# Kernel optimization log

Measured on AMD Instinct MI355X. Metric: run time of the kernel, lower is better.

## Reference

```python
import jax, jax.numpy as jnp
import numpy as np

B, S, D, E, K = 4, 4096, 4096, 64, 2
TEMP = 1.0  # temperature=1.0 -> scale by 1/temperature kept for faithfulness


def setup_inputs() -> dict:
    key = jax.random.key(0)
    k1, k2 = jax.random.split(key)
    x = jax.random.normal(k1, (B, S, D), dtype=jnp.float32)
    W_gate = jax.random.normal(k2, (E, D), dtype=jnp.float32) * (D ** -0.5)
    return {"x": x, "W_gate": W_gate}


def reference(x, W_gate):
    # gate: Linear(d_model, n_experts, bias=False) -> logits [B,S,E]
    logits = jnp.einsum('bsd,ed->bse', x, W_gate)
    # temperature scaling (eval mode: no jitter / expert dropout / gumbel)
    logits = logits * (1.0 / TEMP)
    probs_full = jax.nn.softmax(logits, axis=-1)           # [B,S,E]
    topk_vals, idx = jax.lax.top_k(logits, K)              # [B,S,K]
    scores = jax.nn.softmax(topk_vals, axis=-1)            # renormalized top-k gates
    # z-loss: mean(logsumexp(logits)^2)
    z = jax.nn.logsumexp(logits, axis=-1)                  # [B,S]
    z_loss = jnp.mean(z * z)
    # aux stats (computed under no_grad in the original)
    importance = jax.lax.stop_gradient(jnp.mean(probs_full, axis=(0, 1)))  # [E]
    idx_flat = idx.reshape(-1)
    counts = jnp.zeros((E,), probs_full.dtype).at[idx_flat].add(1.0)       # [E]
    load = jax.lax.stop_gradient(counts / jnp.maximum(jnp.sum(counts), 1.0))
    return (idx, scores, probs_full, z_loss, importance, load)
```

## Files before the change

kernel.cpp:

```cpp
#include <hip/hip_runtime.h>

namespace {
constexpr int D = 4096;
constexpr int E = 64;
constexpr int M = 16384;
constexpr int BM = 64;
constexpr int BK = 64;
constexpr int NT = D / BK;
constexpr int NBLK = M / BM;

constexpr int OFF_IDX = 0;
constexpr int OFF_SCORES = 32768;
constexpr int OFF_PROBS = 65536;
constexpr int OFF_Z = 1114112;
constexpr int OFF_IMP = 1114113;
constexpr int OFF_LOAD = 1114177;

constexpr int WS_STRIDE = 132;
}

__global__ __launch_bounds__(512, 2) void router_fused(
    const float* __restrict__ xg, const float* __restrict__ wg,
    float* __restrict__ out, float* __restrict__ ws) {
  __shared__ float smem[16384];

  const int t = threadIdx.x;
  const int u = t & 127;
  const int s = t >> 7;
  const int tx = u & 15;
  const int ty = u >> 4;
  const int r0 = blockIdx.x * BM;

  const int sr = t >> 3;
  const int sc = (t & 7) * 4;
  const float* xp = xg + (size_t)(r0 + sr) * D + sc;
  const float* wp = wg + (size_t)sr * D + sc;

  float4 vx[2], vw[2];

  auto stage_load = [&](int k0) {
    vx[0] = *(const float4*)(xp + k0);
    vx[1] = *(const float4*)(xp + k0 + 32);
    vw[0] = *(const float4*)(wp + k0);
    vw[1] = *(const float4*)(wp + k0 + 32);
  };
  auto stage_write = [&](float* buf) {
    float* Xs = buf;
    float* Ws = buf + 4096;
#pragma unroll
    for (int h = 0; h < 2; ++h) {
      const int c = sc + h * 32;
      const int sw = ((c >> 4) & 3) << 3;
      const int rp = sr ^ sw;
      Xs[(c + 0) * 64 + rp] = vx[h].x;
      Xs[(c + 1) * 64 + rp] = vx[h].y;
      Xs[(c + 2) * 64 + rp] = vx[h].z;
      Xs[(c + 3) * 64 + rp] = vx[h].w;
      Ws[(c + 0) * 64 + rp] = vw[h].x;
      Ws[(c + 1) * 64 + rp] = vw[h].y;
      Ws[(c + 2) * 64 + rp] = vw[h].z;
      Ws[(c + 3) * 64 + rp] = vw[h].w;
    }
  };

  float acc[8][4];
#pragma unroll
  for (int i = 0; i < 8; ++i)
#pragma unroll
    for (int j = 0; j < 4; ++j) acc[i][j] = 0.f;

  const int rbx = (ty * 8) ^ (s << 3);
  const int rbw = (tx * 4) ^ (s << 3);

  stage_load(0);
  stage_write(smem);

  for (int r = 0; r < NT; ++r) {
    __syncthreads();
    if (r + 1 < NT) stage_load((r + 1) * BK);

    const float* buf = smem + (r & 1) * 8192;
    const float* Xs = buf + (size_t)(s * 16) * 64;
    const float* Ws = buf + 4096 + (size_t)(s * 16) * 64;
#pragma unroll
    for (int kk = 0; kk < 16; ++kk) {
      const float4 a0 = *(const float4*)&Xs[kk * 64 + rbx];
      const float4 a1 = *(const float4*)&Xs[kk * 64 + rbx + 4];
      const float4 bw = *(const float4*)&Ws[kk * 64 + rbw];
      const float av[8] = {a0.x, a0.y, a0.z, a0.w, a1.x, a1.y, a1.z, a1.w};
      const float bv[4] = {bw.x, bw.y, bw.z, bw.w};
#pragma unroll
      for (int i = 0; i < 8; ++i)
#pragma unroll
        for (int j = 0; j < 4; ++j) acc[i][j] = fmaf(av[i], bv[j], acc[i][j]);
    }
    if (r + 1 < NT) stage_write(smem + ((r + 1) & 1) * 8192);
  }

  float* P = smem;
  __syncthreads();
  if (s >= 2) {
    float* p = P + ((size_t)((s - 2) * 128 + u)) * 33;
#pragma unroll
    for (int i = 0; i < 8; ++i)
#pragma unroll
      for (int j = 0; j < 4; ++j) p[i * 4 + j] = acc[i][j];
  }
  __syncthreads();
  if (s < 2) {
    const float* p = P + ((size_t)(s * 128 + u)) * 33;
#pragma unroll
    for (int i = 0; i < 8; ++i)
#pragma unroll
      for (int j = 0; j < 4; ++j) acc[i][j] += p[i * 4 + j];
  }
  __syncthreads();
  if (s == 1) {
    float* p = P + (size_t)u * 33;
#pragma unroll
    for (int i = 0; i < 8; ++i)
#pragma unroll
      for (int j = 0; j < 4; ++j) p[i * 4 + j] = acc[i][j];
  }
  __syncthreads();

  float* Lg = smem + 8448;
  float* rowmax = smem + 12608;
  float* rowrs = rowmax + 64;
  float* zrow = rowrs + 64;
  int* cnt = (int*)(zrow + 64);

  if (s == 0) {
    const float* p = P + (size_t)u * 33;
#pragma unroll
    for (int i = 0; i < 8; ++i)
#pragma unroll
      for (int j = 0; j < 4; ++j) {
        const float v = acc[i][j] + p[i * 4 + j];
        Lg[(ty * 8 + i) * 65 + tx * 4 + j] = v;
      }
  }
  if (t < 64) cnt[t] = 0;
  __syncthreads();

  if (t < 64) {
    const float* row = Lg + t * 65;
    float v1 = -3.402823466e+38f, v2 = -3.402823466e+38f;
    int i1 = 0, i2 = 0;
#pragma unroll 8
    for (int e = 0; e < 64; ++e) {
      const float x = row[e];
      if (x > v1) {
        v2 = v1; i2 = i1; v1 = x; i1 = e;
      } else if (x > v2) {
        v2 = x; i2 = e;
      }
    }
    float ssum = 0.f;
#pragma unroll 8
    for (int e = 0; e < 64; ++e) ssum += __expf(row[e] - v1);
    const float z = v1 + __logf(ssum);
    rowmax[t] = v1;
    rowrs[t] = 1.f / ssum;
    zrow[t] = z * z;

    const int r = r0 + t;
    out[OFF_IDX + 2 * r] = (float)i1;
    out[OFF_IDX + 2 * r + 1] = (float)i2;
    const float e1 = __expf(v2 - v1);
    const float s0 = 1.f / (1.f + e1);
    out[OFF_SCORES + 2 * r] = s0;
    out[OFF_SCORES + 2 * r + 1] = e1 * s0;
    atomicAdd(&cnt[i1], 1);
    atomicAdd(&cnt[i2], 1);
  }
  __syncthreads();

  {
    const int pr = t >> 3;
    const int pc = (t & 7) * 8;
    float* prow = Lg + pr * 65 + pc;
    const float m = rowmax[pr];
    const float rs = rowrs[pr];
    float p[8];
#pragma unroll
    for (int q = 0; q < 8; ++q) p[q] = __expf(prow[q] - m) * rs;
    float4 o0 = {p[0], p[1], p[2], p[3]};
    float4 o1 = {p[4], p[5], p[6], p[7]};
    *(float4*)&out[OFF_PROBS + (size_t)(r0 + pr) * 64 + pc] = o0;
    *(float4*)&out[OFF_PROBS + (size_t)(r0 + pr) * 64 + pc + 4] = o1;
#pragma unroll
    for (int q = 0; q < 8; ++q) prow[q] = p[q];
  }
  __syncthreads();

  if (t < 64) {
    float ic = 0.f;
#pragma unroll 8
    for (int rr = 0; rr < 64; ++rr) ic += Lg[rr * 65 + t];
    ws[(size_t)blockIdx.x * WS_STRIDE + t] = ic;
    ws[(size_t)blockIdx.x * WS_STRIDE + 64 + t] = (float)cnt[t];
    float zz = zrow[t];
#pragma unroll
    for (int off = 32; off > 0; off >>= 1) zz += __shfl_xor(zz, off);
    if (t == 0) ws[(size_t)blockIdx.x * WS_STRIDE + 128] = zz;
  }
}

__global__ __launch_bounds__(192) void router_reduce(
    const float* __restrict__ ws, float* __restrict__ out) {
  const int t = threadIdx.x;
  if (t < 129) {
    float v = 0.f;
#pragma unroll 8
    for (int b = 0; b < NBLK; ++b) v += ws[(size_t)b * WS_STRIDE + t];
    if (t < 64)
      out[OFF_IMP + t] = v * (1.f / 16384.f);
    else if (t < 128)
      out[OFF_LOAD + (t - 64)] = v * (1.f / 32768.f);
    else
      out[OFF_Z] = v * (1.f / 16384.f);
  }
}

extern "C" void kernel_launch(void* const* d_in, const int* in_sizes, int n_in,
                              void* d_out, int out_size, void* d_ws, size_t ws_size,
                              hipStream_t stream) {
  const float* x = (const float*)d_in[0];
  const float* wgate = (const float*)d_in[1];
  float* out = (float*)d_out;
  float* ws = (float*)d_ws;

  router_fused<<<dim3(NBLK), dim3(512), 0, stream>>>(x, wgate, out, ws);
  router_reduce<<<dim3(1), dim3(192), 0, stream>>>(ws, out);
}
```

Baseline: 409.1 us.

## Double BK, use 8x8 per-thread tiles with 8-way split-K and warp-level epilogue

Doubles the K tile to 128 and raises shared memory to 128 KB. Each thread now computes an 8x8 register tile, with eight K-slices reduced through shared memory. This cuts barriers per K step and the LDS traffic per FMA. The epilogue moves to shuffle-based top-2/softmax across 8 lanes per row instead of serial per-row loops, and the final reduce kernel is parallelized across 512 threads. The larger shared memory footprint likely limits blocks per CU below the requested two, lowering occupancy.

```diff
diff --git a/kernel.cpp b/kernel.cpp
--- a/kernel.cpp
+++ b/kernel.cpp
@@ -5,7 +5,7 @@
 constexpr int E = 64;
 constexpr int M = 16384;
 constexpr int BM = 64;
-constexpr int BK = 64;
+constexpr int BK = 128;
 constexpr int NT = D / BK;
 constexpr int NBLK = M / BM;
 
@@ -22,55 +22,47 @@
 __global__ __launch_bounds__(512, 2) void router_fused(
     const float* __restrict__ xg, const float* __restrict__ wg,
     float* __restrict__ out, float* __restrict__ ws) {
-  __shared__ float smem[16384];
+  __shared__ float smem[32768];
 
   const int t = threadIdx.x;
-  const int u = t & 127;
-  const int s = t >> 7;
-  const int tx = u & 15;
-  const int ty = u >> 4;
+  const int u = t & 63;
+  const int s = t >> 6;
+  const int tx = u & 7;
+  const int ty = u >> 3;
   const int r0 = blockIdx.x * BM;
 
   const int sr = t >> 3;
   const int sc = (t & 7) * 4;
   const float* xp = xg + (size_t)(r0 + sr) * D + sc;
   const float* wp = wg + (size_t)sr * D + sc;
-
-  float4 vx[2], vw[2];
-
+  const int rp = sr ^ ((t & 7) << 2);
+
+  float4 vx[4], vw[4];
   auto stage_load = [&](int k0) {
-    vx[0] = *(const float4*)(xp + k0);
-    vx[1] = *(const float4*)(xp + k0 + 32);
-    vw[0] = *(const float4*)(wp + k0);
-    vw[1] = *(const float4*)(wp + k0 + 32);
+#pragma unroll
+    for (int h = 0; h < 4; ++h) {
+      vx[h] = *(const float4*)(xp + k0 + h * 32);
+      vw[h] = *(const float4*)(wp + k0 + h * 32);
+    }
   };
   auto stage_write = [&](float* buf) {
-    float* Xs = buf;
-    float* Ws = buf + 4096;
-#pragma unroll
-    for (int h = 0; h < 2; ++h) {
-      const int c = sc + h * 32;
-      const int sw = ((c >> 4) & 3) << 3;
-      const int rp = sr ^ sw;
-      Xs[(c + 0) * 64 + rp] = vx[h].x;
-      Xs[(c + 1) * 64 + rp] = vx[h].y;
-      Xs[(c + 2) * 64 + rp] = vx[h].z;
-      Xs[(c + 3) * 64 + rp] = vx[h].w;
-      Ws[(c + 0) * 64 + rp] = vw[h].x;
-      Ws[(c + 1) * 64 + rp] = vw[h].y;
-      Ws[(c + 2) * 64 + rp] = vw[h].z;
-      Ws[(c + 3) * 64 + rp] = vw[h].w;
+#pragma unroll
+    for (int h = 0; h < 4; ++h) {
+      float* px = buf + (sc + h * 32) * 64 + rp;
+      px[0] = vx[h].x; px[64] = vx[h].y; px[128] = vx[h].z; px[192] = vx[h].w;
+      float* pw = px + 8192;
+      pw[0] = vw[h].x; pw[64] = vw[h].y; pw[128] = vw[h].z; pw[192] = vw[h].w;
     }
   };
 
-  float acc[8][4];
+  float acc[8][8];
 #pragma unroll
   for (int i = 0; i < 8; ++i)
 #pragma unroll
-    for (int j = 0; j < 4; ++j) acc[i][j] = 0.f;
-
-  const int rbx = (ty * 8) ^ (s << 3);
-  const int rbw = (tx * 4) ^ (s << 3);
+    for (int j = 0; j < 8; ++j) acc[i][j] = 0.f;
+
+  const int rxs = (ty * 8) ^ ((s & 1) << 4);
+  const int rws = (tx * 8) ^ ((s & 1) << 4);
 
   stage_load(0);
   stage_write(smem);
@@ -79,147 +71,181 @@
     __syncthreads();
     if (r + 1 < NT) stage_load((r + 1) * BK);
 
-    const float* buf = smem + (r & 1) * 8192;
-    const float* Xs = buf + (size_t)(s * 16) * 64;
-    const float* Ws = buf + 4096 + (size_t)(s * 16) * 64;
+    const float* buf = smem + (r & 1) * 16384;
+    const float* Xs = buf + s * 1024;
+    const float* Ws = buf + 8192 + s * 1024;
 #pragma unroll
     for (int kk = 0; kk < 16; ++kk) {
-      const float4 a0 = *(const float4*)&Xs[kk * 64 + rbx];
-      const float4 a1 = *(const float4*)&Xs[kk * 64 + rbx + 4];
-      const float4 bw = *(const float4*)&Ws[kk * 64 + rbw];
+      const int vb = (kk >> 2) << 2;
+      const int px = rxs ^ vb;
+      const int pw = rws ^ vb;
+      const float4 a0 = *(const float4*)&Xs[kk * 64 + px];
+      const float4 a1 = *(const float4*)&Xs[kk * 64 + (px ^ 4)];
+      const float4 b0 = *(const float4*)&Ws[kk * 64 + pw];
+      const float4 b1 = *(const float4*)&Ws[kk * 64 + (pw ^ 4)];
       const float av[8] = {a0.x, a0.y, a0.z, a0.w, a1.x, a1.y, a1.z, a1.w};
-      const float bv[4] = {bw.x, bw.y, bw.z, bw.w};
+      const float bv[8] = {b0.x, b0.y, b0.z, b0.w, b1.x, b1.y, b1.z, b1.w};
 #pragma unroll
       for (int i = 0; i < 8; ++i)
 #pragma unroll
-        for (int j = 0; j < 4; ++j) acc[i][j] = fmaf(av[i], bv[j], acc[i][j]);
-    }
-    if (r + 1 < NT) stage_write(smem + ((r + 1) & 1) * 8192);
-  }
-
-  float* P = smem;
-  __syncthreads();
-  if (s >= 2) {
-    float* p = P + ((size_t)((s - 2) * 128 + u)) * 33;
+        for (int j = 0; j < 8; ++j) acc[i][j] = fmaf(av[i], bv[j], acc[i][j]);
+    }
+    if (r + 1 < NT) stage_write(smem + ((r + 1) & 1) * 16384);
+  }
+
+  __syncthreads();
+  {
+    float* P = smem;
+    const int su2 = (s * 64 + u) * 2;
 #pragma unroll
     for (int i = 0; i < 8; ++i)
 #pragma unroll
-      for (int j = 0; j < 4; ++j) p[i * 4 + j] = acc[i][j];
-  }
-  __syncthreads();
-  if (s < 2) {
-    const float* p = P + ((size_t)(s * 128 + u)) * 33;
-#pragma unroll
-    for (int i = 0; i < 8; ++i)
-#pragma unroll
-      for (int j = 0; j < 4; ++j) acc[i][j] += p[i * 4 + j];
-  }
-  __syncthreads();
-  if (s == 1) {
-    float* p = P + (size_t)u * 33;
-#pragma unroll
-    for (int i = 0; i < 8; ++i)
-#pragma unroll
-      for (int j = 0; j < 4; ++j) p[i * 4 + j] = acc[i][j];
-  }
-  __syncthreads();
-
-  float* Lg = smem + 8448;
-  float* rowmax = smem + 12608;
-  float* rowrs = rowmax + 64;
-  float* zrow = rowrs + 64;
-  int* cnt = (int*)(zrow + 64);
-
-  if (s == 0) {
-    const float* p = P + (size_t)u * 33;
-#pragma unroll
-    for (int i = 0; i < 8; ++i)
-#pragma unroll
-      for (int j = 0; j < 4; ++j) {
-        const float v = acc[i][j] + p[i * 4 + j];
-        Lg[(ty * 8 + i) * 65 + tx * 4 + j] = v;
+      for (int jj = 0; jj < 4; ++jj)
+        *(float2*)&P[(i * 4 + jj) * 1024 + su2] =
+            make_float2(acc[i][2 * jj], acc[i][2 * jj + 1]);
+  }
+  __syncthreads();
+
+  float v[8];
+#pragma unroll
+  for (int q = 0; q < 8; ++q) v[q] = 0.f;
+  {
+    const float* P = smem;
+#pragma unroll
+    for (int sl = 0; sl < 8; ++sl)
+#pragma unroll
+      for (int qq = 0; qq < 4; ++qq) {
+        const float2 f =
+            *(const float2*)&P[(s * 4 + qq) * 1024 + (sl * 64 + u) * 2];
+        v[2 * qq] += f.x;
+        v[2 * qq + 1] += f.y;
       }
   }
+  const int row = (u >> 3) * 8 + s;
+  const int ebase = (u & 7) * 8;
+  const int gr = r0 + row;
+
+  __syncthreads();
+  float* PW = smem;
+  float* zw = smem + 512;
+  int* cnt = (int*)(smem + 520);
   if (t < 64) cnt[t] = 0;
   __syncthreads();
 
-  if (t < 64) {
-    const float* row = Lg + t * 65;
-    float v1 = -3.402823466e+38f, v2 = -3.402823466e+38f;
-    int i1 = 0, i2 = 0;
-#pragma unroll 8
-    for (int e = 0; e < 64; ++e) {
-      const float x = row[e];
-      if (x > v1) {
-        v2 = v1; i2 = i1; v1 = x; i1 = e;
-      } else if (x > v2) {
-        v2 = x; i2 = e;
-      }
-    }
-    float ssum = 0.f;
-#pragma unroll 8
-    for (int e = 0; e < 64; ++e) ssum += __expf(row[e] - v1);
-    const float z = v1 + __logf(ssum);
-    rowmax[t] = v1;
-    rowrs[t] = 1.f / ssum;
-    zrow[t] = z * z;
-
-    const int r = r0 + t;
-    out[OFF_IDX + 2 * r] = (float)i1;
-    out[OFF_IDX + 2 * r + 1] = (float)i2;
+  float v1 = v[0]; int i1 = ebase;
+  float v2 = -3.402823466e+38f; int i2 = 0;
+#pragma unroll
+  for (int q = 1; q < 8; ++q) {
+    const float x = v[q];
+    if (x > v1) { v2 = v1; i2 = i1; v1 = x; i1 = ebase + q; }
+    else if (x > v2) { v2 = x; i2 = ebase + q; }
+  }
+#pragma unroll
+  for (int m = 1; m <= 4; m <<= 1) {
+    const float o1 = __shfl_xor(v1, m);
+    const int oi1 = __shfl_xor(i1, m);
+    const float o2 = __shfl_xor(v2, m);
+    const int oi2 = __shfl_xor(i2, m);
+    if (o1 > v1 || (o1 == v1 && oi1 < i1)) {
+      const bool c2 = (o2 > v1) || (o2 == v1 && oi2 < i1);
+      v2 = c2 ? o2 : v1; i2 = c2 ? oi2 : i1;
+      v1 = o1; i1 = oi1;
+    } else if (o1 > v2 || (o1 == v2 && oi1 < i2)) {
+      v2 = o1; i2 = oi1;
+    }
+  }
+
+  float p[8];
+  float ssum = 0.f;
+#pragma unroll
+  for (int q = 0; q < 8; ++q) { p[q] = __expf(v[q] - v1); ssum += p[q]; }
+#pragma unroll
+  for (int m = 1; m <= 4; m <<= 1) ssum += __shfl_xor(ssum, m);
+  const float rs = 1.f / ssum;
+#pragma unroll
+  for (int q = 0; q < 8; ++q) p[q] *= rs;
+
+  {
+    const float4 o0 = {p[0], p[1], p[2], p[3]};
+    const float4 o1 = {p[4], p[5], p[6], p[7]};
+    *(float4*)&out[OFF_PROBS + (size_t)gr * 64 + ebase] = o0;
+    *(float4*)&out[OFF_PROBS + (size_t)gr * 64 + ebase + 4] = o1;
+  }
+  const float z = v1 + __logf(ssum);
+  const float z2 = z * z;
+
+  if ((u & 7) == 0) {
+    out[OFF_IDX + 2 * gr] = (float)i1;
+    out[OFF_IDX + 2 * gr + 1] = (float)i2;
     const float e1 = __expf(v2 - v1);
     const float s0 = 1.f / (1.f + e1);
-    out[OFF_SCORES + 2 * r] = s0;
-    out[OFF_SCORES + 2 * r + 1] = e1 * s0;
+    out[OFF_SCORES + 2 * gr] = s0;
+    out[OFF_SCORES + 2 * gr + 1] = e1 * s0;
     atomicAdd(&cnt[i1], 1);
     atomicAdd(&cnt[i2], 1);
   }
-  __syncthreads();
-
-  {
-    const int pr = t >> 3;
-    const int pc = (t & 7) * 8;
-    float* prow = Lg + pr * 65 + pc;
-    const float m = rowmax[pr];
-    const float rs = rowrs[pr];
-    float p[8];
-#pragma unroll
-    for (int q = 0; q < 8; ++q) p[q] = __expf(prow[q] - m) * rs;
-    float4 o0 = {p[0], p[1], p[2], p[3]};
-    float4 o1 = {p[4], p[5], p[6], p[7]};
-    *(float4*)&out[OFF_PROBS + (size_t)(r0 + pr) * 64 + pc] = o0;
-    *(float4*)&out[OFF_PROBS + (size_t)(r0 + pr) * 64 + pc + 4] = o1;
-#pragma unroll
-    for (int q = 0; q < 8; ++q) prow[q] = p[q];
+
+  float cs[8];
+#pragma unroll
+  for (int q = 0; q < 8; ++q) cs[q] = p[q];
+#pragma unroll
+  for (int m = 8; m <= 32; m <<= 1)
+#pragma unroll
+    for (int q = 0; q < 8; ++q) cs[q] += __shfl_xor(cs[q], m);
+  float zs = z2;
+#pragma unroll
+  for (int m = 8; m <= 32; m <<= 1) zs += __shfl_xor(zs, m);
+  if (u < 8) {
+    const float4 c0 = {cs[0], cs[1], cs[2], cs[3]};
+    const float4 c1 = {cs[4], cs[5], cs[6], cs[7]};
+    *(float4*)&PW[s * 64 + u * 8] = c0;
+    *(float4*)&PW[s * 64 + u * 8 + 4] = c1;
+    if (u == 0) zw[s] = zs;
   }
   __syncthreads();
 
   if (t < 64) {
     float ic = 0.f;
-#pragma unroll 8
-    for (int rr = 0; rr < 64; ++rr) ic += Lg[rr * 65 + t];
+#pragma unroll
+    for (int w = 0; w < 8; ++w) ic += PW[w * 64 + t];
     ws[(size_t)blockIdx.x * WS_STRIDE + t] = ic;
     ws[(size_t)blockIdx.x * WS_STRIDE + 64 + t] = (float)cnt[t];
-    float zz = zrow[t];
-#pragma unroll
-    for (int off = 32; off > 0; off >>= 1) zz += __shfl_xor(zz, off);
-    if (t == 0) ws[(size_t)blockIdx.x * WS_STRIDE + 128] = zz;
-  }
-}
-
-__global__ __launch_bounds__(192) void router_reduce(
+  } else if (t == 64) {
+    float zz = 0.f;
+#pragma unroll
+    for (int w = 0; w < 8; ++w) zz += zw[w];
+    ws[(size_t)blockIdx.x * WS_STRIDE + 128] = zz;
+  }
+}
+
+__global__ __launch_bounds__(512) void router_reduce(
     const float* __restrict__ ws, float* __restrict__ out) {
+  __shared__ float part[4][128];
+  __shared__ float zp[4];
   const int t = threadIdx.x;
-  if (t < 129) {
-    float v = 0.f;
+  const int c = t >> 7;
+  const int slot = t & 127;
+  float v = 0.f;
 #pragma unroll 8
-    for (int b = 0; b < NBLK; ++b) v += ws[(size_t)b * WS_STRIDE + t];
+  for (int i = 0; i < 64; ++i)
+    v += ws[(size_t)(c * 64 + i) * WS_STRIDE + slot];
+  part[c][slot] = v;
+  if (t < 4) {
+    float zz = 0.f;
+#pragma unroll 8
+    for (int i = 0; i < 64; ++i)
+      zz += ws[(size_t)(t * 64 + i) * WS_STRIDE + 128];
+    zp[t] = zz;
+  }
+  __syncthreads();
+  if (t < 128) {
+    const float s4 = part[0][t] + part[1][t] + part[2][t] + part[3][t];
     if (t < 64)
-      out[OFF_IMP + t] = v * (1.f / 16384.f);
-    else if (t < 128)
-      out[OFF_LOAD + (t - 64)] = v * (1.f / 32768.f);
+      out[OFF_IMP + t] = s4 * (1.f / 16384.f);
     else
-      out[OFF_Z] = v * (1.f / 16384.f);
+      out[OFF_LOAD + (t - 64)] = s4 * (1.f / 32768.f);
+  } else if (t == 128) {
+    out[OFF_Z] = (zp[0] + zp[1] + zp[2] + zp[3]) * (1.f / 16384.f);
   }
 }
 
@@ -232,5 +258,5 @@
   float* ws = (float*)d_ws;
 
   router_fused<<<dim3(NBLK), dim3(512), 0, stream>>>(x, wgate, out, ws);
-  router_reduce<<<dim3(1), dim3(192), 0, stream>>>(ws, out);
-}
+  router_reduce<<<dim3(1), dim3(512), 0, stream>>>(ws, out);
+}
```

Result: slower. 1.152 ms (+181.6%).
